# Performance work log

Hardware: AMD Instinct MI355X
Metric: run time of the kernel (lower is better)

The kernel has to match this reference:

```python
import jax, jax.numpy as jnp
import numpy as np

N = 50000   # nodes
E = 800000  # edges
F = 64      # node_feature_dim
H = 128     # hidden_dim


def setup_inputs() -> dict:
    key = jax.random.key(0)
    ks = jax.random.split(key, 20)
    def w(k, shape, fan_in):
        return jax.random.normal(k, shape, jnp.float32) / np.sqrt(fan_in)
    return {
        "x": jax.random.normal(ks[0], (N, F), jnp.float32),
        "edge_index": jax.random.randint(ks[1], (2, E), 0, N, jnp.int32),
        "enc_w1": w(ks[2], (F, H), F), "enc_b1": jnp.zeros((H,), jnp.float32),
        "enc_w2": w(ks[3], (H, H), H), "enc_b2": jnp.zeros((H,), jnp.float32),
        "w_c1": w(ks[4], (H, H), H), "b_c1": jnp.zeros((H,), jnp.float32),
        "w_c2": w(ks[5], (H, H), H), "b_c2": jnp.zeros((H,), jnp.float32),
        "w_c3": w(ks[6], (H, H), H), "b_c3": jnp.zeros((H,), jnp.float32),
        "dec_w1": w(ks[7], (H, H), H), "dec_b1": jnp.zeros((H,), jnp.float32),
        "dec_w2": w(ks[8], (H, F), H), "dec_b2": jnp.zeros((F,), jnp.float32),
    }


def _gcn_conv(h, W, b, src, dst, dinv):
    # PyG GCNConv: D^-1/2 (A+I) D^-1/2 (h W) + b  (self-loops already in src/dst)
    hw = h @ W                                   # [N, H]
    norm = dinv[src] * dinv[dst]                 # [E+N]
    msg = hw[src] * norm[:, None]                # gather + scale
    return jax.ops.segment_sum(msg, dst, num_segments=N) + b


def reference(x, edge_index, enc_w1, enc_b1, enc_w2, enc_b2,
              w_c1, b_c1, w_c2, b_c2, w_c3, b_c3,
              dec_w1, dec_b1, dec_w2, dec_b2):
    loop = jnp.arange(N, dtype=edge_index.dtype)
    src = jnp.concatenate([edge_index[0], loop])
    dst = jnp.concatenate([edge_index[1], loop])
    deg = jax.ops.segment_sum(jnp.ones_like(dst, jnp.float32), dst, num_segments=N)
    dinv = jax.lax.rsqrt(deg)  # deg >= 1 because of self-loops

    h = jax.nn.relu(x @ enc_w1 + enc_b1) @ enc_w2 + enc_b2  # encoder MLP
    h = jax.nn.relu(_gcn_conv(h, w_c1, b_c1, src, dst, dinv))
    h = jax.nn.relu(_gcn_conv(h, w_c2, b_c2, src, dst, dinv))
    h = jax.nn.relu(_gcn_conv(h, w_c3, b_c3, src, dst, dinv))
    # window_size == 1: chunk+cat is identity
    out = jax.nn.relu(h @ dec_w1 + dec_b1) @ dec_w2 + dec_b2  # decoder MLP
    return jax.nn.sigmoid(out)
```

## Files before the change

### kernel.cpp

```cpp
#include <hip/hip_runtime.h>
#include <stdint.h>

#define NN 50000
#define NE 800000
#define FD 64
#define HD 128
#define NBKT 196
#define BCAP 5120
#define P1E 4096

typedef __attribute__((ext_vector_type(8))) short short8;
typedef __attribute__((ext_vector_type(4))) float f32x4;

#define AS1 __attribute__((address_space(1)))
#define AS3 __attribute__((address_space(3)))

__device__ __forceinline__ float bflo(unsigned int v) {
    union { unsigned int u; float f; } c; c.u = v << 16; return c.f;
}
__device__ __forceinline__ float bfhi(unsigned int v) {
    union { unsigned int u; float f; } c; c.u = v & 0xffff0000u; return c.f;
}
__device__ __forceinline__ unsigned short f2bf(float f) {
    union { float f; unsigned int u; } c; c.f = f;
    unsigned int u = c.u;
    return (unsigned short)((u + 0x7fffu + ((u >> 16) & 1u)) >> 16);
}
__device__ __forceinline__ unsigned int pack2(float a, float b) {
    return (unsigned int)f2bf(a) | ((unsigned int)f2bf(b) << 16);
}

__global__ void wt_k(const float* __restrict__ w0, const float* __restrict__ w1,
                     const float* __restrict__ w2, const float* __restrict__ w3,
                     const float* __restrict__ w4, const float* __restrict__ w5,
                     const float* __restrict__ w6,
                     unsigned short* __restrict__ t0, unsigned short* __restrict__ t1,
                     unsigned short* __restrict__ t2, unsigned short* __restrict__ t3,
                     unsigned short* __restrict__ t4, unsigned short* __restrict__ t5,
                     unsigned short* __restrict__ t6)
{
    int b = blockIdx.x;
    const float* W; unsigned short* T; int K, C;
    if      (b <  32) { W = w0; T = t0; K =  64; C = 128; }
    else if (b <  96) { W = w1; T = t1; K = 128; C = 128; b -= 32; }
    else if (b < 160) { W = w2; T = t2; K = 128; C = 128; b -= 96; }
    else if (b < 224) { W = w3; T = t3; K = 128; C = 128; b -= 160; }
    else if (b < 288) { W = w4; T = t4; K = 128; C = 128; b -= 224; }
    else if (b < 352) { W = w5; T = t5; K = 128; C = 128; b -= 288; }
    else              { W = w6; T = t6; K = 128; C =  64; b -= 352; }
    int e = b * 256 + threadIdx.x;
    int k, c;
    if (C == 128) { k = e >> 7; c = e & 127; } else { k = e >> 6; c = e & 63; }
    int gmask = (K >> 3) - 1;
    int gsw = (k >> 3) ^ (c & gmask);
    T[c * K + gsw * 8 + (k & 7)] = f2bf(W[e]);
}

__global__ void scanB_k(const int* __restrict__ gcnt, int* __restrict__ bsum, int nb) {
    __shared__ int sh[256];
    int t = threadIdx.x;
    int v = (t < nb) ? gcnt[t] : 0;
    sh[t] = v; __syncthreads();
    for (int d = 1; d < 256; d <<= 1) {
        int x = (t >= d) ? sh[t - d] : 0; __syncthreads();
        sh[t] += x; __syncthreads();
    }
    if (t < nb) bsum[t] = sh[t] - v;
}

template <int K, int COLS, int EPI, bool BIAS, bool RSCALE, bool A_F32, bool OUT_F32>
__device__ __forceinline__ void mgemm_dev(
    int bid,
    const void* __restrict__ Av,
    const unsigned short* __restrict__ Wt,
    const float* __restrict__ bias,
    const float* __restrict__ dinv,
    void* __restrict__ outv, int nrows)
{
    constexpr int NB = COLS / 16;
    constexpr int KC = K / 32;
    constexpr int GMASK = (K >> 3) - 1;
    __shared__ __align__(16) unsigned char Ws8[COLS * K * 2];

    const int tid = threadIdx.x;
    const int wave = tid >> 6;
    const int lane = tid & 63;

    {
        constexpr int ROUNDS = COLS * K * 2 / 4096;
        const int gb = wave * 1024 + lane * 16;
        const int lb = wave * 1024;
        #pragma unroll
        for (int r = 0; r < ROUNDS; r++) {
            __builtin_amdgcn_global_load_lds(
                (const AS1 unsigned int*)((const unsigned char*)Wt + r * 4096 + gb),
                (AS3 unsigned int*)(Ws8 + r * 4096 + lb),
                16, 0, 0);
        }
    }

    const int m = lane & 15;
    const int q = lane >> 4;
    const int row0 = bid * 64 + wave * 16;

    f32x4 acc[NB];
    #pragma unroll
    for (int i = 0; i < NB; i++) acc[i] = (f32x4){0.f, 0.f, 0.f, 0.f};

    const bool arow_ok = !A_F32 || (row0 + m) < nrows;

    short8 af[KC];
    #pragma unroll
    for (int kc = 0; kc < KC; kc++) {
        if constexpr (A_F32) {
            const float* arowf = (const float*)Av + (size_t)(row0 + m) * K + q * 8 + kc * 32;
            float4 lo = make_float4(0.f, 0.f, 0.f, 0.f), hi = lo;
            if (arow_ok) { lo = *(const float4*)arowf; hi = *(const float4*)(arowf + 4); }
            af[kc][0] = (short)f2bf(lo.x); af[kc][1] = (short)f2bf(lo.y);
            af[kc][2] = (short)f2bf(lo.z); af[kc][3] = (short)f2bf(lo.w);
            af[kc][4] = (short)f2bf(hi.x); af[kc][5] = (short)f2bf(hi.y);
            af[kc][6] = (short)f2bf(hi.z); af[kc][7] = (short)f2bf(hi.w);
        } else {
            const unsigned short* arow = (const unsigned short*)Av + (size_t)(row0 + m) * K + q * 8 + kc * 32;
            af[kc] = *(const short8*)arow;
        }
    }
    __syncthreads();

    #pragma unroll
    for (int kc = 0; kc < KC; kc++) {
        #pragma unroll
        for (int nb = 0; nb < NB; nb++) {
            const int c = nb * 16 + m;
            const int gsw = (kc * 4 + q) ^ (c & GMASK);
            short8 bf = *(const short8*)&Ws8[(c * K + gsw * 8) * 2];
            acc[nb] = __builtin_amdgcn_mfma_f32_16x16x32_bf16(af[kc], bf, acc[nb], 0, 0, 0);
        }
    }

    float bv[NB];
    #pragma unroll
    for (int nb = 0; nb < NB; nb++) bv[nb] = BIAS ? bias[nb * 16 + m] : 0.f;

    #pragma unroll
    for (int r = 0; r < 4; r++) {
        int row = row0 + q * 4 + r;
        if (row < nrows) {
            float sc = RSCALE ? dinv[row] : 1.f;
            #pragma unroll
            for (int nb = 0; nb < NB; nb++) {
                float t = acc[nb][r];
                if (RSCALE) t *= sc;
                t += bv[nb];
                if (EPI == 1) t = fmaxf(t, 0.f);
                if (EPI == 2) t = 1.f / (1.f + __expf(-t));
                if constexpr (OUT_F32) {
                    ((float*)outv)[(size_t)row * COLS + nb * 16 + m] = t;
                } else {
                    ((unsigned short*)outv)[(size_t)row * COLS + nb * 16 + m] = f2bf(t);
                }
            }
        }
    }
}

template <int K, int COLS, int EPI, bool BIAS, bool RSCALE, bool A_F32, bool OUT_F32>
__global__ __launch_bounds__(256) void mgemm_k(
    const void* __restrict__ Av, const unsigned short* __restrict__ Wt,
    const float* __restrict__ bias, const float* __restrict__ dinv,
    void* __restrict__ outv, int nrows)
{
    mgemm_dev<K, COLS, EPI, BIAS, RSCALE, A_F32, OUT_F32>(blockIdx.x, Av, Wt, bias, dinv, outv, nrows);
}

__global__ __launch_bounds__(256) void k1_k(
    const float* __restrict__ x, const unsigned short* __restrict__ t0,
    const float* __restrict__ enc_b1, unsigned short* __restrict__ bufA,
    const int* __restrict__ src, const int* __restrict__ dst,
    int* __restrict__ gcnt, unsigned int* __restrict__ bucket, int gb)
{
    if ((int)blockIdx.x < gb) {
        mgemm_dev<64, 128, 1, true, false, true, false>(blockIdx.x, x, t0, enc_b1, nullptr, bufA, NN);
    } else {
        __shared__ int lcnt[256], lsw[256], lexc[256], lofs[256], lrank[256];
        __shared__ unsigned int stage[P1E];
        const int tid = threadIdx.x;
        const int bb = blockIdx.x - gb;
        lcnt[tid] = 0; lrank[tid] = 0;
        __syncthreads();
        unsigned int ent[P1E / 256];
        #pragma unroll
        for (int u = 0; u < P1E / 256; u++) {
            int g = bb * P1E + u * 256 + tid;
            if (g < NE) {
                int d = dst[g], s = src[g];
                int bk = d >> 8;
                atomicAdd(&lcnt[bk], 1);
                ent[u] = (unsigned int)s | ((unsigned int)(d & 255) << 16)
                       | ((unsigned int)bk << 24);
            } else ent[u] = 0xFFFFFFFFu;
        }
        __syncthreads();
        int v = lcnt[tid];
        lsw[tid] = v; __syncthreads();
        for (int d = 1; d < 256; d <<= 1) {
            int xx = (tid >= d) ? lsw[tid - d] : 0; __syncthreads();
            lsw[tid] += xx; __syncthreads();
        }
        lexc[tid] = lsw[tid] - v;
        lofs[tid] = (v > 0) ? atomicAdd(&gcnt[tid], v) : 0;
        __syncthreads();
        #pragma unroll
        for (int u = 0; u < P1E / 256; u++) {
            if (ent[u] != 0xFFFFFFFFu) {
                int bk = ent[u] >> 24;
                int r = atomicAdd(&lrank[bk], 1);
                stage[lexc[bk] + r] = ent[u];
            }
        }
        __syncthreads();
        int cb = NE - bb * P1E; if (cb > P1E) cb = P1E;
        for (int i = tid; i < cb; i += 256) {
            unsigned int e = stage[i];
            int bk = e >> 24;
            bucket[(size_t)bk * BCAP + lofs[bk] + (i - lexc[bk])] = e;
        }
    }
}

__global__ __launch_bounds__(256) void k2_k(
    const unsigned short* __restrict__ bufA, const unsigned short* __restrict__ t1,
    const float* __restrict__ enc_b2, unsigned short* __restrict__ bufB,
    const int* __restrict__ gcnt, const unsigned int* __restrict__ bucket,
    const int* __restrict__ bsum,
    int* __restrict__ off, float* __restrict__ dinv,
    unsigned short* __restrict__ csr, int gb)
{
    if ((int)blockIdx.x < gb) {
        mgemm_dev<128, 128, 0, true, false, false, false>(blockIdx.x, bufA, t1, enc_b2, nullptr, bufB, NN);
    } else {
        __shared__ int lc[256], sw[256], sexc[256], lr[256];
        const int tid = threadIdx.x;
        const int b = blockIdx.x - gb;
        const int cb = gcnt[b];
        unsigned int ent[BCAP / 256];
        #pragma unroll
        for (int u = 0; u < BCAP / 256; u++) {
            int i = u * 256 + tid;
            ent[u] = (i < cb) ? bucket[(size_t)b * BCAP + i] : 0xFFFFFFFFu;
        }
        lc[tid] = 0; lr[tid] = 0;
        __syncthreads();
        #pragma unroll
        for (int u = 0; u < BCAP / 256; u++)
            if (ent[u] != 0xFFFFFFFFu) atomicAdd(&lc[(ent[u] >> 16) & 255], 1);
        __syncthreads();
        int v = lc[tid];
        int node = b * 256 + tid;
        if (node < NN) dinv[node] = rsqrtf((float)(v + 1));
        sw[tid] = v; __syncthreads();
        for (int d = 1; d < 256; d <<= 1) {
            int xx = (tid >= d) ? sw[tid - d] : 0; __syncthreads();
            sw[tid] += xx; __syncthreads();
        }
        sexc[tid] = sw[tid] - v;
        if (node < NN) off[node] = sexc[tid];
        __syncthreads();
        const int base = bsum[b];
        #pragma unroll
        for (int u = 0; u < BCAP / 256; u++) {
            if (ent[u] != 0xFFFFFFFFu) {
                int dl = (ent[u] >> 16) & 255;
                int r = atomicAdd(&lr[dl], 1);
                csr[base + sexc[dl] + r] = (unsigned short)(ent[u] & 0xffff);
            }
        }
    }
}

__global__ __launch_bounds__(256) void agg_k(
    const uint2* __restrict__ hws,
    const int* __restrict__ off, const int* __restrict__ bsum,
    const unsigned short* __restrict__ csr,
    const float* __restrict__ dinv, const float* __restrict__ bias,
    uint2* __restrict__ out, int n)
{
    int node = blockIdx.x * 8 + (threadIdx.x >> 5);
    if (node >= n) return;
    int lane = threadIdx.x & 31;

    uint2 v = hws[node * 32 + lane];
    float s0 = bflo(v.x), s1 = bfhi(v.x), s2 = bflo(v.y), s3 = bfhi(v.y);

    int b = off[node] + bsum[node >> 8];
    int e = (node + 1 < n) ? (off[node + 1] + bsum[(node + 1) >> 8]) : NE;
    int j = b;
    for (; j + 8 <= e; j += 8) {
        uint2 t[8];
        #pragma unroll
        for (int u = 0; u < 8; u++) t[u] = hws[(int)csr[j + u] * 32 + lane];
        #pragma unroll
        for (int u = 0; u < 8; u++) {
            s0 += bflo(t[u].x); s1 += bfhi(t[u].x);
            s2 += bflo(t[u].y); s3 += bfhi(t[u].y);
        }
    }
    for (; j < e; j++) {
        uint2 t = hws[(int)csr[j] * 32 + lane];
        s0 += bflo(t.x); s1 += bfhi(t.x);
        s2 += bflo(t.y); s3 += bfhi(t.y);
    }

    float di = dinv[node];
    float4 bv = *(const float4*)(bias + 4 * lane);
    float r0 = fmaxf(fmaf(di, s0, bv.x), 0.f);
    float r1 = fmaxf(fmaf(di, s1, bv.y), 0.f);
    float r2 = fmaxf(fmaf(di, s2, bv.z), 0.f);
    float r3 = fmaxf(fmaf(di, s3, bv.w), 0.f);
    uint2 o; o.x = pack2(r0, r1); o.y = pack2(r2, r3);
    out[node * 32 + lane] = o;
}

extern "C" void kernel_launch(void* const* d_in, const int* in_sizes, int n_in,
                              void* d_out, int out_size, void* d_ws, size_t ws_size,
                              hipStream_t stream)
{
    const float* x      = (const float*)d_in[0];
    const int*   ei     = (const int*)d_in[1];
    const float* enc_w1 = (const float*)d_in[2];
    const float* enc_b1 = (const float*)d_in[3];
    const float* enc_w2 = (const float*)d_in[4];
    const float* enc_b2 = (const float*)d_in[5];
    const float* w_c1   = (const float*)d_in[6];
    const float* b_c1   = (const float*)d_in[7];
    const float* w_c2   = (const float*)d_in[8];
    const float* b_c2   = (const float*)d_in[9];
    const float* w_c3   = (const float*)d_in[10];
    const float* b_c3   = (const float*)d_in[11];
    const float* dec_w1 = (const float*)d_in[12];
    const float* dec_b1 = (const float*)d_in[13];
    const float* dec_w2 = (const float*)d_in[14];
    const float* dec_b2 = (const float*)d_in[15];

    const int* src = ei;
    const int* dst = ei + NE;

    const int NP = 50048;

    char* ws = (char*)d_ws;
    size_t o = 0;
    auto alloc = [&](size_t bytes) -> void* {
        void* p = ws + o;
        o = (o + bytes + 255) & ~(size_t)255;
        return p;
    };
    int*   gcnt = (int*)alloc(256 * 4);
    int*   off  = (int*)alloc((size_t)(NN + 1) * 4);
    int*   bsum = (int*)alloc(256 * 4);
    unsigned short* csr = (unsigned short*)alloc((size_t)NE * 2);
    unsigned int* bucket = (unsigned int*)alloc((size_t)NBKT * BCAP * 4);
    float* dinv = (float*)alloc((size_t)NN * 4);
    unsigned short* bufA = (unsigned short*)alloc((size_t)NP * HD * 2);
    unsigned short* bufB = (unsigned short*)alloc((size_t)NP * HD * 2);
    unsigned short* t0 = (unsigned short*)alloc(64 * 128 * 2);
    unsigned short* t1 = (unsigned short*)alloc(128 * 128 * 2);
    unsigned short* t2 = (unsigned short*)alloc(128 * 128 * 2);
    unsigned short* t3 = (unsigned short*)alloc(128 * 128 * 2);
    unsigned short* t4 = (unsigned short*)alloc(128 * 128 * 2);
    unsigned short* t5 = (unsigned short*)alloc(128 * 128 * 2);
    unsigned short* t6 = (unsigned short*)alloc(128 * 64 * 2);
    (void)ws_size; (void)n_in; (void)in_sizes; (void)out_size;

    hipMemsetAsync(gcnt, 0, 256 * 4, stream);

    const int PB = (NE + P1E - 1) / P1E;
    const int GB = NP / 64;
    const int AB = (NN + 7) / 8;

    wt_k<<<384, 256, 0, stream>>>(enc_w1, enc_w2, w_c1, w_c2, w_c3, dec_w1, dec_w2,
                                  t0, t1, t2, t3, t4, t5, t6);
    k1_k<<<GB + PB, 256, 0, stream>>>(x, t0, enc_b1, bufA, src, dst, gcnt, bucket, GB);
    scanB_k<<<1, 256, 0, stream>>>(gcnt, bsum, NBKT);
    k2_k<<<GB + NBKT, 256, 0, stream>>>(bufA, t1, enc_b2, bufB, gcnt, bucket, bsum,
                                        off, dinv, csr, GB);
    mgemm_k<128, 128, 0, false, true, false, false><<<GB, 256, 0, stream>>>(bufB, t2, nullptr, dinv, bufA, NN);
    agg_k<<<AB, 256, 0, stream>>>((const uint2*)bufA, off, bsum, csr, dinv, b_c1, (uint2*)bufB, NN);
    mgemm_k<128, 128, 0, false, true, false, false><<<GB, 256, 0, stream>>>(bufB, t3, nullptr, dinv, bufA, NN);
    agg_k<<<AB, 256, 0, stream>>>((const uint2*)bufA, off, bsum, csr, dinv, b_c2, (uint2*)bufB, NN);
    mgemm_k<128, 128, 0, false, true, false, false><<<GB, 256, 0, stream>>>(bufB, t4, nullptr, dinv, bufA, NN);
    agg_k<<<AB, 256, 0, stream>>>((const uint2*)bufA, off, bsum, csr, dinv, b_c3, (uint2*)bufB, NN);
    mgemm_k<128, 128, 1, true, false, false, false><<<GB, 256, 0, stream>>>(bufB, t5, dec_b1, nullptr, bufA, NN);
    mgemm_k<128, 64, 2, true, false, false, true><<<GB, 256, 0, stream>>>(bufA, t6, dec_b2, nullptr, d_out, NN);
}
```

Baseline: 281.1 us.

## Fold weight transposes and bucket scan into neighboring kernels, drop scan launch

```diff
diff --git a/kernel.cpp b/kernel.cpp
--- a/kernel.cpp
+++ b/kernel.cpp
@@ -7,7 +7,7 @@
 #define HD 128
 #define NBKT 196
 #define BCAP 5120
-#define P1E 4096
+#define P1E 8192
 
 typedef __attribute__((ext_vector_type(8))) short short8;
 typedef __attribute__((ext_vector_type(4))) float f32x4;
@@ -30,42 +30,11 @@
     return (unsigned int)f2bf(a) | ((unsigned int)f2bf(b) << 16);
 }
 
-__global__ void wt_k(const float* __restrict__ w0, const float* __restrict__ w1,
-                     const float* __restrict__ w2, const float* __restrict__ w3,
-                     const float* __restrict__ w4, const float* __restrict__ w5,
-                     const float* __restrict__ w6,
-                     unsigned short* __restrict__ t0, unsigned short* __restrict__ t1,
-                     unsigned short* __restrict__ t2, unsigned short* __restrict__ t3,
-                     unsigned short* __restrict__ t4, unsigned short* __restrict__ t5,
-                     unsigned short* __restrict__ t6)
-{
-    int b = blockIdx.x;
-    const float* W; unsigned short* T; int K, C;
-    if      (b <  32) { W = w0; T = t0; K =  64; C = 128; }
-    else if (b <  96) { W = w1; T = t1; K = 128; C = 128; b -= 32; }
-    else if (b < 160) { W = w2; T = t2; K = 128; C = 128; b -= 96; }
-    else if (b < 224) { W = w3; T = t3; K = 128; C = 128; b -= 160; }
-    else if (b < 288) { W = w4; T = t4; K = 128; C = 128; b -= 224; }
-    else if (b < 352) { W = w5; T = t5; K = 128; C = 128; b -= 288; }
-    else              { W = w6; T = t6; K = 128; C =  64; b -= 352; }
-    int e = b * 256 + threadIdx.x;
-    int k, c;
-    if (C == 128) { k = e >> 7; c = e & 127; } else { k = e >> 6; c = e & 63; }
-    int gmask = (K >> 3) - 1;
-    int gsw = (k >> 3) ^ (c & gmask);
-    T[c * K + gsw * 8 + (k & 7)] = f2bf(W[e]);
-}
-
-__global__ void scanB_k(const int* __restrict__ gcnt, int* __restrict__ bsum, int nb) {
-    __shared__ int sh[256];
-    int t = threadIdx.x;
-    int v = (t < nb) ? gcnt[t] : 0;
-    sh[t] = v; __syncthreads();
-    for (int d = 1; d < 256; d <<= 1) {
-        int x = (t >= d) ? sh[t - d] : 0; __syncthreads();
-        sh[t] += x; __syncthreads();
-    }
-    if (t < nb) bsum[t] = sh[t] - v;
+__global__ void wt0_k(const float* __restrict__ w0, unsigned short* __restrict__ t0) {
+    int e = blockIdx.x * 256 + threadIdx.x;
+    int k = e >> 7, c = e & 127;
+    int gsw = (k >> 3) ^ (c & 7);
+    t0[c * 64 + gsw * 8 + (k & 7)] = f2bf(w0[e]);
 }
 
 template <int K, int COLS, int EPI, bool BIAS, bool RSCALE, bool A_F32, bool OUT_F32>
@@ -174,18 +143,26 @@
 }
 
 __global__ __launch_bounds__(256) void k1_k(
-    const float* __restrict__ x, const unsigned short* __restrict__ t0,
+    const float* __restrict__ x, const unsigned short* __restrict__ t0s,
     const float* __restrict__ enc_b1, unsigned short* __restrict__ bufA,
     const int* __restrict__ src, const int* __restrict__ dst,
-    int* __restrict__ gcnt, unsigned int* __restrict__ bucket, int gb)
-{
-    if ((int)blockIdx.x < gb) {
-        mgemm_dev<64, 128, 1, true, false, true, false>(blockIdx.x, x, t0, enc_b1, nullptr, bufA, NN);
-    } else {
+    int* __restrict__ gcnt, unsigned int* __restrict__ bucket,
+    const float* __restrict__ w1, const float* __restrict__ w2,
+    const float* __restrict__ w3, const float* __restrict__ w4,
+    const float* __restrict__ w5, const float* __restrict__ w6,
+    unsigned short* __restrict__ t1, unsigned short* __restrict__ t2,
+    unsigned short* __restrict__ t3, unsigned short* __restrict__ t4,
+    unsigned short* __restrict__ t5, unsigned short* __restrict__ t6,
+    int gb, int pb)
+{
+    const int b = blockIdx.x;
+    if (b < gb) {
+        mgemm_dev<64, 128, 1, true, false, true, false>(b, x, t0s, enc_b1, nullptr, bufA, NN);
+    } else if (b < gb + pb) {
         __shared__ int lcnt[256], lsw[256], lexc[256], lofs[256], lrank[256];
         __shared__ unsigned int stage[P1E];
         const int tid = threadIdx.x;
-        const int bb = blockIdx.x - gb;
+        const int bb = b - gb;
         lcnt[tid] = 0; lrank[tid] = 0;
         __syncthreads();
         unsigned int ent[P1E / 256];
@@ -225,6 +202,20 @@
             int bk = e >> 24;
             bucket[(size_t)bk * BCAP + lofs[bk] + (i - lexc[bk])] = e;
         }
+    } else {
+        int b2 = b - gb - pb;
+        const float* W; unsigned short* T; int C = 128;
+        if      (b2 <  64) { W = w1; T = t1; }
+        else if (b2 < 128) { W = w2; T = t2; b2 -= 64; }
+        else if (b2 < 192) { W = w3; T = t3; b2 -= 128; }
+        else if (b2 < 256) { W = w4; T = t4; b2 -= 192; }
+        else if (b2 < 320) { W = w5; T = t5; b2 -= 256; }
+        else               { W = w6; T = t6; b2 -= 320; C = 64; }
+        int e = b2 * 256 + threadIdx.x;
+        int k, c;
+        if (C == 128) { k = e >> 7; c = e & 127; } else { k = e >> 6; c = e & 63; }
+        int gsw = (k >> 3) ^ (c & 15);
+        T[c * 128 + gsw * 8 + (k & 7)] = f2bf(W[e]);
     }
 }
 
@@ -232,17 +223,23 @@
     const unsigned short* __restrict__ bufA, const unsigned short* __restrict__ t1,
     const float* __restrict__ enc_b2, unsigned short* __restrict__ bufB,
     const int* __restrict__ gcnt, const unsigned int* __restrict__ bucket,
-    const int* __restrict__ bsum,
     int* __restrict__ off, float* __restrict__ dinv,
     unsigned short* __restrict__ csr, int gb)
 {
     if ((int)blockIdx.x < gb) {
         mgemm_dev<128, 128, 0, true, false, false, false>(blockIdx.x, bufA, t1, enc_b2, nullptr, bufB, NN);
     } else {
-        __shared__ int lc[256], sw[256], sexc[256], lr[256];
+        __shared__ int lc[256], sw[256], sexc[256], lr[256], gsh[256];
         const int tid = threadIdx.x;
         const int b = blockIdx.x - gb;
+        int gv = (tid < NBKT) ? gcnt[tid] : 0;
+        gsh[tid] = gv; __syncthreads();
+        for (int d = 1; d < 256; d <<= 1) {
+            int xx = (tid >= d) ? gsh[tid - d] : 0; __syncthreads();
+            gsh[tid] += xx; __syncthreads();
+        }
         const int cb = gcnt[b];
+        const int base = gsh[b] - cb;
         unsigned int ent[BCAP / 256];
         #pragma unroll
         for (int u = 0; u < BCAP / 256; u++) {
@@ -264,9 +261,9 @@
             sw[tid] += xx; __syncthreads();
         }
         sexc[tid] = sw[tid] - v;
-        if (node < NN) off[node] = sexc[tid];
-        __syncthreads();
-        const int base = bsum[b];
+        if (node < NN) off[node] = base + sexc[tid];
+        if (b == NBKT - 1 && tid == 0) off[NN] = NE;
+        __syncthreads();
         #pragma unroll
         for (int u = 0; u < BCAP / 256; u++) {
             if (ent[u] != 0xFFFFFFFFu) {
@@ -280,7 +277,7 @@
 
 __global__ __launch_bounds__(256) void agg_k(
     const uint2* __restrict__ hws,
-    const int* __restrict__ off, const int* __restrict__ bsum,
+    const int* __restrict__ off,
     const unsigned short* __restrict__ csr,
     const float* __restrict__ dinv, const float* __restrict__ bias,
     uint2* __restrict__ out, int n)
@@ -292,8 +289,7 @@
     uint2 v = hws[node * 32 + lane];
     float s0 = bflo(v.x), s1 = bfhi(v.x), s2 = bflo(v.y), s3 = bfhi(v.y);
 
-    int b = off[node] + bsum[node >> 8];
-    int e = (node + 1 < n) ? (off[node + 1] + bsum[(node + 1) >> 8]) : NE;
+    int b = off[node], e = off[node + 1];
     int j = b;
     for (; j + 8 <= e; j += 8) {
         uint2 t[8];
@@ -356,7 +352,6 @@
     };
     int*   gcnt = (int*)alloc(256 * 4);
     int*   off  = (int*)alloc((size_t)(NN + 1) * 4);
-    int*   bsum = (int*)alloc(256 * 4);
     unsigned short* csr = (unsigned short*)alloc((size_t)NE * 2);
     unsigned int* bucket = (unsigned int*)alloc((size_t)NBKT * BCAP * 4);
     float* dinv = (float*)alloc((size_t)NN * 4);
@@ -377,18 +372,18 @@
     const int GB = NP / 64;
     const int AB = (NN + 7) / 8;
 
-    wt_k<<<384, 256, 0, stream>>>(enc_w1, enc_w2, w_c1, w_c2, w_c3, dec_w1, dec_w2,
-                                  t0, t1, t2, t3, t4, t5, t6);
-    k1_k<<<GB + PB, 256, 0, stream>>>(x, t0, enc_b1, bufA, src, dst, gcnt, bucket, GB);
-    scanB_k<<<1, 256, 0, stream>>>(gcnt, bsum, NBKT);
-    k2_k<<<GB + NBKT, 256, 0, stream>>>(bufA, t1, enc_b2, bufB, gcnt, bucket, bsum,
+    wt0_k<<<32, 256, 0, stream>>>(enc_w1, t0);
+    k1_k<<<GB + PB + 352, 256, 0, stream>>>(x, t0, enc_b1, bufA, src, dst, gcnt, bucket,
+                                            enc_w2, w_c1, w_c2, w_c3, dec_w1, dec_w2,
+                                            t1, t2, t3, t4, t5, t6, GB, PB);
+    k2_k<<<GB + NBKT, 256, 0, stream>>>(bufA, t1, enc_b2, bufB, gcnt, bucket,
                                         off, dinv, csr, GB);
     mgemm_k<128, 128, 0, false, true, false, false><<<GB, 256, 0, stream>>>(bufB, t2, nullptr, dinv, bufA, NN);
-    agg_k<<<AB, 256, 0, stream>>>((const uint2*)bufA, off, bsum, csr, dinv, b_c1, (uint2*)bufB, NN);
+    agg_k<<<AB, 256, 0, stream>>>((const uint2*)bufA, off, csr, dinv, b_c1, (uint2*)bufB, NN);
     mgemm_k<128, 128, 0, false, true, false, false><<<GB, 256, 0, stream>>>(bufB, t3, nullptr, dinv, bufA, NN);
-    agg_k<<<AB, 256, 0, stream>>>((const uint2*)bufA, off, bsum, csr, dinv, b_c2, (uint2*)bufB, NN);
+    agg_k<<<AB, 256, 0, stream>>>((const uint2*)bufA, off, csr, dinv, b_c2, (uint2*)bufB, NN);
     mgemm_k<128, 128, 0, false, true, false, false><<<GB, 256, 0, stream>>>(bufB, t4, nullptr, dinv, bufA, NN);
-    agg_k<<<AB, 256, 0, stream>>>((const uint2*)bufA, off, bsum, csr, dinv, b_c3, (uint2*)bufB, NN);
+    agg_k<<<AB, 256, 0, stream>>>((const uint2*)bufA, off, csr, dinv, b_c3, (uint2*)bufB, NN);
     mgemm_k<128, 128, 1, true, false, false, false><<<GB, 256, 0, stream>>>(bufB, t5, dec_b1, nullptr, bufA, NN);
     mgemm_k<128, 64, 2, true, false, false, true><<<GB, 256, 0, stream>>>(bufA, t6, dec_b2, nullptr, d_out, NN);
 }
```

After: 280.7 us. Within noise of the previous version (-0.1%).
